# Performance work log

Hardware: AMD Instinct MI355X
Metric: run time of the kernel (lower is better)

## Reference

```python
import jax, jax.numpy as jnp
import numpy as np

D_MODEL = 1024
NUM_HEADS = 16
D_K = D_MODEL // NUM_HEADS
SCALE = float(np.sqrt(D_K))


def setup_inputs() -> dict:
    key = jax.random.key(0)
    ks = jax.random.split(key, 11)
    B, S, D = 2, 2048, D_MODEL
    def lin(kw):
        # xavier-uniform-ish weight, zero bias (matches torch init style)
        lim = float(np.sqrt(6.0 / (D + D)))
        return jax.random.uniform(kw, (D, D), jnp.float32, -lim, lim)
    return {
        "q": jax.random.normal(ks[0], (B, S, D), jnp.float32),
        "k": jax.random.normal(ks[1], (B, S, D), jnp.float32),
        "v": jax.random.normal(ks[2], (B, S, D), jnp.float32),
        "Wq": lin(ks[3]), "bq": jnp.zeros((D,), jnp.float32),
        "Wk": lin(ks[4]), "bk": jnp.zeros((D,), jnp.float32),
        "Wv": lin(ks[5]), "bv": jnp.zeros((D,), jnp.float32),
        "Wo": lin(ks[6]), "bo": jnp.zeros((D,), jnp.float32),
    }


def _split_heads(x):
    B, S, _ = x.shape
    return x.reshape(B, S, NUM_HEADS, D_K).transpose(0, 2, 1, 3)  # (B,H,S,dk)


def reference(q, k, v, Wq, bq, Wk, bk, Wv, bv, Wo, bo):
    # torch nn.Linear: y = x @ W.T + b
    Q = _split_heads(q @ Wq.T + bq)
    K = _split_heads(k @ Wk.T + bk)
    V = _split_heads(v @ Wv.T + bv)
    scores = jnp.einsum("bhqd,bhkd->bhqk", Q, K) / SCALE
    # numerically-stable softmax with detached max (as in the torch code)
    m = jax.lax.stop_gradient(jnp.max(scores, axis=-1, keepdims=True))
    exp_scores = jnp.exp(scores - m)
    attn = exp_scores / (jnp.sum(exp_scores, axis=-1, keepdims=True) + 1e-9)
    out = jnp.einsum("bhqk,bhkd->bhqd", attn, V)  # (B,H,S,dk)
    B, H, S, dk = out.shape
    out = out.transpose(0, 2, 1, 3).reshape(B, S, H * dk)
    return out @ Wo.T + bo
```

## Files before the change

### kernel.cpp

```cpp
#include <hip/hip_runtime.h>


#define D_MODEL 1024
#define NHEADS  16
#define DKH     64
#define SEQ     2048
#define BATCH   2
#define MTOT    (BATCH * SEQ)
#define XE      ((long)MTOT * D_MODEL)
#define WE      ((long)D_MODEL * D_MODEL)
#define QSCALE  0.18033688011112042f

typedef __attribute__((ext_vector_type(8))) short short8v;
typedef __attribute__((ext_vector_type(4))) short short4v;
typedef __attribute__((ext_vector_type(4))) float f32x4;

typedef __attribute__((address_space(1))) void as1_void;
typedef __attribute__((address_space(3))) void as3_void;

__device__ __forceinline__ void gload16(const void* g, void* l) {
    __builtin_amdgcn_global_load_lds((const as1_void*)g, (as3_void*)l, 16, 0, 0);
}

__device__ __forceinline__ unsigned short f2bf(float x) {
    unsigned int u = __float_as_uint(x);
    u += 0x7FFFu + ((u >> 16) & 1u);
    return (unsigned short)(u >> 16);
}

__device__ __forceinline__ float fexp2(float x) {
    return __builtin_amdgcn_exp2f(x);
}

__device__ __forceinline__ unsigned int cvt_pk_bf16(float lo, float hi) {
    unsigned int r;
    asm("v_cvt_pk_bf16_f32 %0, %1, %2" : "=v"(r) : "v"(lo), "v"(hi));
    return r;
}

__device__ __forceinline__ int swz_u(int row, int col) {
    int byte = (col << 1) ^ ((row & 7) << 4);
    return (row << 6) + (byte >> 1);
}

__device__ __forceinline__ int swz_v(int d, int kv) {
    int slot = (d & 6) | ((d >> 3) & 1);
    int byte = (kv << 1) ^ (slot << 4);
    return (d << 6) + (byte >> 1);
}

struct ConvArgs {
    const float*    src[7];
    unsigned short* dst[7];
    int             n4[7];
};

__global__ __launch_bounds__(256) void convert_kernel(ConvArgs a) {
    int z = blockIdx.y;
    const float4*   s = (const float4*)a.src[z];
    unsigned short* d = a.dst[z];
    int n = a.n4[z];
    for (int i = blockIdx.x * blockDim.x + threadIdx.x; i < n;
         i += gridDim.x * blockDim.x) {
        float4 v = s[i];
        ushort4 o;
        o.x = f2bf(v.x); o.y = f2bf(v.y); o.z = f2bf(v.z); o.w = f2bf(v.w);
        *(ushort4*)(d + 4L * i) = o;
    }
}

__device__ __forceinline__ void stv(float* p, float v)          { *p = v; }
__device__ __forceinline__ void stv(unsigned short* p, float v) { *p = f2bf(v); }

template <typename OutT>
__device__ __forceinline__ void gemm_core(const unsigned short* __restrict__ A,
                                          const unsigned short* __restrict__ Bm,
                                          const float* __restrict__ bias,
                                          OutT* __restrict__ C,
                                          int K, int N, float scale) {
    __shared__ unsigned short As[128 * 32];
    __shared__ unsigned short Bs[128 * 32];

    const int t    = threadIdx.x;
    const int lane = t & 63;
    const int w    = t >> 6;
    const int wm   = w >> 1, wn = w & 1;
    const int l15  = lane & 15, g = lane >> 4;
    const long m0  = (long)blockIdx.y * 128;
    const long n0  = (long)blockIdx.x * 128;

    f32x4 acc[4][4] = {};

    const int idx0 = t, idx1 = t + 256;
    const int r0 = idx0 >> 2, c0 = (idx0 & 3) * 8;
    const int r1 = idx1 >> 2, c1 = (idx1 & 3) * 8;
    const unsigned short* pa0 = A  + (m0 + r0) * K + c0;
    const unsigned short* pa1 = A  + (m0 + r1) * K + c1;
    const unsigned short* pb0 = Bm + (n0 + r0) * K + c0;
    const unsigned short* pb1 = Bm + (n0 + r1) * K + c1;

    for (int k0 = 0; k0 < K; k0 += 32) {
        gload16(pa0 + k0, &As[idx0 * 8]);
        gload16(pa1 + k0, &As[idx1 * 8]);
        gload16(pb0 + k0, &Bs[idx0 * 8]);
        gload16(pb1 + k0, &Bs[idx1 * 8]);
        __syncthreads();

        short8v af[4], bf_[4];
#pragma unroll
        for (int mf = 0; mf < 4; ++mf)
            af[mf] = *(const short8v*)&As[(wm * 64 + mf * 16 + l15) * 32 + g * 8];
#pragma unroll
        for (int nf = 0; nf < 4; ++nf)
            bf_[nf] = *(const short8v*)&Bs[(wn * 64 + nf * 16 + l15) * 32 + g * 8];
#pragma unroll
        for (int mf = 0; mf < 4; ++mf)
#pragma unroll
            for (int nf = 0; nf < 4; ++nf)
                acc[mf][nf] = __builtin_amdgcn_mfma_f32_16x16x32_bf16(
                    af[mf], bf_[nf], acc[mf][nf], 0, 0, 0);
        __syncthreads();
    }

    float bvv[4];
#pragma unroll
    for (int nf = 0; nf < 4; ++nf)
        bvv[nf] = bias[n0 + wn * 64 + nf * 16 + l15];

#pragma unroll
    for (int mf = 0; mf < 4; ++mf)
#pragma unroll
        for (int nf = 0; nf < 4; ++nf)
#pragma unroll
            for (int r = 0; r < 4; ++r) {
                long row = m0 + wm * 64 + mf * 16 + g * 4 + r;
                long col = n0 + wn * 64 + nf * 16 + l15;
                float v = (acc[mf][nf][r] + bvv[nf]) * scale;
                stv(C + row * (long)N + col, v);
            }
}

__global__ __launch_bounds__(256) void proj_kernel(
    const unsigned short* __restrict__ xb, const unsigned short* __restrict__ wb,
    const float* __restrict__ bq, const float* __restrict__ bk,
    const float* __restrict__ bv, unsigned short* __restrict__ qkv) {
    int z = blockIdx.z;
    const float* bias = (z == 0) ? bq : (z == 1) ? bk : bv;
    float scale = (z == 0) ? QSCALE : 1.0f;
    gemm_core<unsigned short>(xb + (long)z * XE, wb + (long)z * WE, bias,
                              qkv + (long)z * XE, D_MODEL, D_MODEL, scale);
}

__global__ __launch_bounds__(256) void out_kernel(
    const unsigned short* __restrict__ ob, const unsigned short* __restrict__ wo,
    const float* __restrict__ bo, float* __restrict__ out) {
    gemm_core<float>(ob, wo, bo, out, D_MODEL, D_MODEL, 1.0f);
}

#define KVB 4096

__global__ __launch_bounds__(512) void attn_kernel(
    const unsigned short* __restrict__ Qb, const unsigned short* __restrict__ Kb,
    const unsigned short* __restrict__ Vb, unsigned short* __restrict__ Ob) {
    __shared__ alignas(16) unsigned short Ks[2 * KVB];
    __shared__ alignas(16) unsigned short Vt[2 * KVB];
    __shared__ alignas(16) unsigned short Ps[8][16 * 64];
    __shared__ alignas(16) float corrS[8][16];

    const int t = threadIdx.x, lane = t & 63, w = t >> 6;
    const int l15 = lane & 15, g = lane >> 4;
    const int bh = blockIdx.y;
    const long headoff = (long)(bh >> 4) * SEQ * D_MODEL + (long)(bh & 15) * DKH;
    const int q0w = blockIdx.x * 128 + w * 16;

    short8v qf[2];
#pragma unroll
    for (int ks = 0; ks < 2; ++ks)
        qf[ks] = *(const short8v*)(Qb + headoff +
            (long)(q0w + l15) * D_MODEL + ks * 32 + g * 8);

    short8v onesv;
#pragma unroll
    for (int j = 0; j < 8; ++j) onesv[j] = (short)0x3F80;

    f32x4 o[4] = {};
    f32x4 ol = {};
    float mrun = -3.0e38f;

    const int vd0  = (t & 31) * 2;
    const int vkv0 = (t >> 5) * 4;
    const int kr0 = t >> 3, ks0 = t & 7;

    unsigned int va[4];

#define ISSUE_V(kt)                                                        \
    _Pragma("unroll")                                                      \
    for (int j = 0; j < 4; ++j)                                            \
        va[j] = *(const unsigned int*)(Vb + headoff +                      \
            (long)((kt) + vkv0 + j) * D_MODEL + vd0);

#define ISSUE_K(kt, off)                                                   \
    gload16(Kb + headoff + (long)((kt) + kr0) * D_MODEL +                  \
                ((ks0 ^ (kr0 & 7)) << 3), &Ks[(off) + t * 8]);

#define WRITE_V(off)                                                       \
    {                                                                      \
        short4v ra, rb;                                                    \
        _Pragma("unroll")                                                  \
        for (int j = 0; j < 4; ++j) {                                      \
            ra[j] = (short)(va[j] & 0xffffu);                              \
            rb[j] = (short)(va[j] >> 16);                                  \
        }                                                                  \
        *(short4v*)&Vt[(off) + swz_v(vd0,     vkv0)] = ra;                 \
        *(short4v*)&Vt[(off) + swz_v(vd0 + 1, vkv0)] = rb;                 \
    }

    asm volatile("s_waitcnt vmcnt(0)" ::: "memory");
    ISSUE_V(0);
    ISSUE_K(0, 0);
    WRITE_V(0);
    int cur = 0;

    for (int it = 0; it < SEQ / 64; ++it) {
        const int nxt = cur ^ 1;
        const int ktn = (((it + 1) & (SEQ / 64 - 1))) * 64;
        ISSUE_V(ktn);
        ISSUE_K(ktn, nxt * KVB);
        asm volatile("s_waitcnt vmcnt(5)" ::: "memory");
        asm volatile("s_waitcnt lgkmcnt(0)" ::: "memory");
        __builtin_amdgcn_sched_barrier(0);
        __builtin_amdgcn_s_barrier();
        __builtin_amdgcn_sched_barrier(0);

        const int kO = cur * KVB;

        f32x4 st[4] = {};
        __builtin_amdgcn_s_setprio(1);
#pragma unroll
        for (int ks = 0; ks < 2; ++ks)
#pragma unroll
            for (int mf = 0; mf < 4; ++mf) {
                short8v kf = *(const short8v*)&Ks[kO + swz_u(mf * 16 + l15, ks * 32 + g * 8)];
                st[mf] = __builtin_amdgcn_mfma_f32_16x16x32_bf16(
                    kf, qf[ks], st[mf], 0, 0, 0);
            }
        __builtin_amdgcn_s_setprio(0);

        float vmax = st[0][0];
#pragma unroll
        for (int mf = 0; mf < 4; ++mf)
#pragma unroll
            for (int r = 0; r < 4; ++r)
                vmax = fmaxf(vmax, st[mf][r]);
        vmax = fmaxf(vmax, __shfl_xor(vmax, 16));
        vmax = fmaxf(vmax, __shfl_xor(vmax, 32));

        const bool grow = __any(vmax > mrun + 8.0f);
        if (grow) {
            float mnew = fmaxf(mrun, vmax);
            float corr = fexp2(mrun - mnew);
            mrun = mnew;
            if (g == 0) corrS[w][l15] = corr;
        }

#pragma unroll
        for (int mf = 0; mf < 4; ++mf)
#pragma unroll
            for (int r = 0; r < 4; ++r)
                st[mf][r] = fexp2(st[mf][r] - mrun);

        unsigned short* Pw = Ps[w];
#pragma unroll
        for (int mf = 0; mf < 4; ++mf) {
            uint2 pk;
            pk.x = cvt_pk_bf16(st[mf][0], st[mf][1]);
            pk.y = cvt_pk_bf16(st[mf][2], st[mf][3]);
            *(uint2*)&Pw[swz_u(l15, mf * 16 + g * 4)] = pk;
        }

        if (grow) {
            float4 cv = *(const float4*)&corrS[w][g * 4];
#pragma unroll
            for (int nd = 0; nd < 4; ++nd)
#pragma unroll
                for (int r = 0; r < 4; ++r)
                    o[nd][r] *= cv[r];
#pragma unroll
            for (int r = 0; r < 4; ++r) ol[r] *= cv[r];
        }

        __builtin_amdgcn_s_setprio(1);
#pragma unroll
        for (int ks2 = 0; ks2 < 2; ++ks2) {
            short8v pf = *(const short8v*)&Pw[swz_u(l15, ks2 * 32 + g * 8)];
            ol = __builtin_amdgcn_mfma_f32_16x16x32_bf16(
                pf, onesv, ol, 0, 0, 0);
#pragma unroll
            for (int nd = 0; nd < 4; ++nd) {
                short8v vf = *(const short8v*)&Vt[kO + swz_v(nd * 16 + l15, ks2 * 32 + g * 8)];
                o[nd] = __builtin_amdgcn_mfma_f32_16x16x32_bf16(
                    pf, vf, o[nd], 0, 0, 0);
            }
        }
        __builtin_amdgcn_s_setprio(0);

        WRITE_V(nxt * KVB);
        cur = nxt;
    }

#pragma unroll
    for (int r = 0; r < 4; ++r) {
        float inv = 1.f / (ol[r] + 1e-9f);
        long rowoff = headoff + (long)(q0w + g * 4 + r) * D_MODEL;
#pragma unroll
        for (int nd = 0; nd < 4; ++nd)
            Ob[rowoff + nd * 16 + l15] = f2bf(o[nd][r] * inv);
    }
#undef ISSUE_V
#undef ISSUE_K
#undef WRITE_V
}

extern "C" void kernel_launch(void* const* d_in, const int* in_sizes, int n_in,
                              void* d_out, int out_size, void* d_ws, size_t ws_size,
                              hipStream_t stream) {
    unsigned short* ws  = (unsigned short*)d_ws;
    unsigned short* xb  = ws;
    unsigned short* wb  = ws + 3L * XE;
    unsigned short* qkv = ws + 3L * XE + 4L * WE;
    unsigned short* ob  = qkv + 3L * XE;

    ConvArgs ca;
    ca.src[0] = (const float*)d_in[0]; ca.dst[0] = xb;           ca.n4[0] = (int)(XE / 4);
    ca.src[1] = (const float*)d_in[1]; ca.dst[1] = xb + XE;      ca.n4[1] = (int)(XE / 4);
    ca.src[2] = (const float*)d_in[2]; ca.dst[2] = xb + 2L * XE; ca.n4[2] = (int)(XE / 4);
    ca.src[3] = (const float*)d_in[3]; ca.dst[3] = wb;           ca.n4[3] = (int)(WE / 4);
    ca.src[4] = (const float*)d_in[5]; ca.dst[4] = wb + WE;      ca.n4[4] = (int)(WE / 4);
    ca.src[5] = (const float*)d_in[7]; ca.dst[5] = wb + 2L * WE; ca.n4[5] = (int)(WE / 4);
    ca.src[6] = (const float*)d_in[9]; ca.dst[6] = wb + 3L * WE; ca.n4[6] = (int)(WE / 4);

    hipLaunchKernelGGL(convert_kernel, dim3(512, 7), dim3(256), 0, stream, ca);

    hipLaunchKernelGGL(proj_kernel, dim3(8, 32, 3), dim3(256), 0, stream,
                       xb, wb, (const float*)d_in[4], (const float*)d_in[6],
                       (const float*)d_in[8], qkv);

    hipLaunchKernelGGL(attn_kernel, dim3(16, 32), dim3(512), 0, stream,
                       qkv, qkv + XE, qkv + 2L * XE, ob);

    hipLaunchKernelGGL(out_kernel, dim3(8, 32), dim3(256), 0, stream,
                       ob, wb + 3L * WE, (const float*)d_in[10], (float*)d_out);
}
```

Baseline: 140.9 us.

## Switch attention to 32x32x16 MFMA with 32-row waves and permlane P reuse

Rewrites the attention kernel around 32x32x16 bf16 MFMA tiles. Each wave now owns 32 query rows and the block drops to 256 threads. The P matrix no longer makes a round trip through LDS: it is rearranged in registers with v_permlane32_swap and fed straight into the PV MFMA, which also removes the Ps shared buffer. The goal is fewer LDS transactions and higher MFMA throughput per wave, at the cost of more accumulator registers and fewer waves per block to hide latency.

```diff
diff --git a/kernel.cpp b/kernel.cpp
--- a/kernel.cpp
+++ b/kernel.cpp
@@ -11,9 +11,10 @@
 #define WE      ((long)D_MODEL * D_MODEL)
 #define QSCALE  0.18033688011112042f
 
-typedef __attribute__((ext_vector_type(8))) short short8v;
-typedef __attribute__((ext_vector_type(4))) short short4v;
-typedef __attribute__((ext_vector_type(4))) float f32x4;
+typedef __attribute__((ext_vector_type(8)))  short short8v;
+typedef __attribute__((ext_vector_type(4)))  short short4v;
+typedef __attribute__((ext_vector_type(4)))  float f32x4;
+typedef __attribute__((ext_vector_type(16))) float f32x16;
 
 typedef __attribute__((address_space(1))) void as1_void;
 typedef __attribute__((address_space(3))) void as3_void;
@@ -159,60 +160,62 @@
 
 #define KVB 4096
 
-__global__ __launch_bounds__(512) void attn_kernel(
+__global__ __launch_bounds__(256) void attn_kernel(
     const unsigned short* __restrict__ Qb, const unsigned short* __restrict__ Kb,
     const unsigned short* __restrict__ Vb, unsigned short* __restrict__ Ob) {
     __shared__ alignas(16) unsigned short Ks[2 * KVB];
     __shared__ alignas(16) unsigned short Vt[2 * KVB];
-    __shared__ alignas(16) unsigned short Ps[8][16 * 64];
-    __shared__ alignas(16) float corrS[8][16];
+    __shared__ alignas(16) float corrS[4][32];
 
     const int t = threadIdx.x, lane = t & 63, w = t >> 6;
-    const int l15 = lane & 15, g = lane >> 4;
+    const int l31 = lane & 31, h = lane >> 5;
     const int bh = blockIdx.y;
     const long headoff = (long)(bh >> 4) * SEQ * D_MODEL + (long)(bh & 15) * DKH;
-    const int q0w = blockIdx.x * 128 + w * 16;
-
-    short8v qf[2];
-#pragma unroll
-    for (int ks = 0; ks < 2; ++ks)
-        qf[ks] = *(const short8v*)(Qb + headoff +
-            (long)(q0w + l15) * D_MODEL + ks * 32 + g * 8);
+    const int q0w = blockIdx.x * 128 + w * 32;
+
+    short8v qf[4];
+#pragma unroll
+    for (int step = 0; step < 4; ++step)
+        qf[step] = *(const short8v*)(Qb + headoff +
+            (long)(q0w + l31) * D_MODEL + step * 16 + h * 8);
 
     short8v onesv;
 #pragma unroll
     for (int j = 0; j < 8; ++j) onesv[j] = (short)0x3F80;
 
-    f32x4 o[4] = {};
-    f32x4 ol = {};
+    f32x16 o[2] = {};
+    f32x16 ol = {};
     float mrun = -3.0e38f;
 
     const int vd0  = (t & 31) * 2;
-    const int vkv0 = (t >> 5) * 4;
-    const int kr0 = t >> 3, ks0 = t & 7;
-
-    unsigned int va[4];
+    const int vkv0 = (t >> 5) * 8;
+    const int kr0 = t >> 3,         ks0  = t & 7;
+    const int kr1 = (t + 256) >> 3, ks1_ = (t + 256) & 7;
+
+    unsigned int va[8];
 
 #define ISSUE_V(kt)                                                        \
     _Pragma("unroll")                                                      \
-    for (int j = 0; j < 4; ++j)                                            \
+    for (int j = 0; j < 8; ++j)                                            \
         va[j] = *(const unsigned int*)(Vb + headoff +                      \
             (long)((kt) + vkv0 + j) * D_MODEL + vd0);
 
 #define ISSUE_K(kt, off)                                                   \
     gload16(Kb + headoff + (long)((kt) + kr0) * D_MODEL +                  \
-                ((ks0 ^ (kr0 & 7)) << 3), &Ks[(off) + t * 8]);
+                ((ks0 ^ (kr0 & 7)) << 3), &Ks[(off) + t * 8]);             \
+    gload16(Kb + headoff + (long)((kt) + kr1) * D_MODEL +                  \
+                ((ks1_ ^ (kr1 & 7)) << 3), &Ks[(off) + (t + 256) * 8]);
 
 #define WRITE_V(off)                                                       \
     {                                                                      \
-        short4v ra, rb;                                                    \
+        short8v ra, rb;                                                    \
         _Pragma("unroll")                                                  \
-        for (int j = 0; j < 4; ++j) {                                      \
+        for (int j = 0; j < 8; ++j) {                                      \
             ra[j] = (short)(va[j] & 0xffffu);                              \
             rb[j] = (short)(va[j] >> 16);                                  \
         }                                                                  \
-        *(short4v*)&Vt[(off) + swz_v(vd0,     vkv0)] = ra;                 \
-        *(short4v*)&Vt[(off) + swz_v(vd0 + 1, vkv0)] = rb;                 \
+        *(short8v*)&Vt[(off) + swz_v(vd0,     vkv0)] = ra;                 \
+        *(short8v*)&Vt[(off) + swz_v(vd0 + 1, vkv0)] = rb;                 \
     }
 
     asm volatile("s_waitcnt vmcnt(0)" ::: "memory");
@@ -223,10 +226,10 @@
 
     for (int it = 0; it < SEQ / 64; ++it) {
         const int nxt = cur ^ 1;
-        const int ktn = (((it + 1) & (SEQ / 64 - 1))) * 64;
+        const int ktn = ((it + 1) & (SEQ / 64 - 1)) * 64;
         ISSUE_V(ktn);
         ISSUE_K(ktn, nxt * KVB);
-        asm volatile("s_waitcnt vmcnt(5)" ::: "memory");
+        asm volatile("s_waitcnt vmcnt(10)" ::: "memory");
         asm volatile("s_waitcnt lgkmcnt(0)" ::: "memory");
         __builtin_amdgcn_sched_barrier(0);
         __builtin_amdgcn_s_barrier();
@@ -234,25 +237,23 @@
 
         const int kO = cur * KVB;
 
-        f32x4 st[4] = {};
+        f32x16 st[2] = {};
         __builtin_amdgcn_s_setprio(1);
 #pragma unroll
-        for (int ks = 0; ks < 2; ++ks)
-#pragma unroll
-            for (int mf = 0; mf < 4; ++mf) {
-                short8v kf = *(const short8v*)&Ks[kO + swz_u(mf * 16 + l15, ks * 32 + g * 8)];
-                st[mf] = __builtin_amdgcn_mfma_f32_16x16x32_bf16(
-                    kf, qf[ks], st[mf], 0, 0, 0);
-            }
+        for (int step = 0; step < 4; ++step) {
+            short8v kf0 = *(const short8v*)&Ks[kO + swz_u(l31,      step * 16 + h * 8)];
+            st[0] = __builtin_amdgcn_mfma_f32_32x32x16_bf16(kf0, qf[step], st[0], 0, 0, 0);
+            short8v kf1 = *(const short8v*)&Ks[kO + swz_u(32 + l31, step * 16 + h * 8)];
+            st[1] = __builtin_amdgcn_mfma_f32_32x32x16_bf16(kf1, qf[step], st[1], 0, 0, 0);
+        }
         __builtin_amdgcn_s_setprio(0);
 
         float vmax = st[0][0];
 #pragma unroll
-        for (int mf = 0; mf < 4; ++mf)
-#pragma unroll
-            for (int r = 0; r < 4; ++r)
-                vmax = fmaxf(vmax, st[mf][r]);
-        vmax = fmaxf(vmax, __shfl_xor(vmax, 16));
+        for (int b = 0; b < 2; ++b)
+#pragma unroll
+            for (int r = 0; r < 16; ++r)
+                vmax = fmaxf(vmax, st[b][r]);
         vmax = fmaxf(vmax, __shfl_xor(vmax, 32));
 
         const bool grow = __any(vmax > mrun + 8.0f);
@@ -260,48 +261,47 @@
             float mnew = fmaxf(mrun, vmax);
             float corr = fexp2(mrun - mnew);
             mrun = mnew;
-            if (g == 0) corrS[w][l15] = corr;
+            if (lane < 32) corrS[w][l31] = corr;
         }
 
 #pragma unroll
-        for (int mf = 0; mf < 4; ++mf)
-#pragma unroll
-            for (int r = 0; r < 4; ++r)
-                st[mf][r] = fexp2(st[mf][r] - mrun);
-
-        unsigned short* Pw = Ps[w];
-#pragma unroll
-        for (int mf = 0; mf < 4; ++mf) {
-            uint2 pk;
-            pk.x = cvt_pk_bf16(st[mf][0], st[mf][1]);
-            pk.y = cvt_pk_bf16(st[mf][2], st[mf][3]);
-            *(uint2*)&Pw[swz_u(l15, mf * 16 + g * 4)] = pk;
-        }
+        for (int b = 0; b < 2; ++b)
+#pragma unroll
+            for (int r = 0; r < 16; ++r)
+                st[b][r] = fexp2(st[b][r] - mrun);
 
         if (grow) {
-            float4 cv = *(const float4*)&corrS[w][g * 4];
-#pragma unroll
-            for (int nd = 0; nd < 4; ++nd)
-#pragma unroll
-                for (int r = 0; r < 4; ++r)
-                    o[nd][r] *= cv[r];
-#pragma unroll
-            for (int r = 0; r < 4; ++r) ol[r] *= cv[r];
-        }
-
-        __builtin_amdgcn_s_setprio(1);
-#pragma unroll
-        for (int ks2 = 0; ks2 < 2; ++ks2) {
-            short8v pf = *(const short8v*)&Pw[swz_u(l15, ks2 * 32 + g * 8)];
-            ol = __builtin_amdgcn_mfma_f32_16x16x32_bf16(
-                pf, onesv, ol, 0, 0, 0);
-#pragma unroll
-            for (int nd = 0; nd < 4; ++nd) {
-                short8v vf = *(const short8v*)&Vt[kO + swz_v(nd * 16 + l15, ks2 * 32 + g * 8)];
-                o[nd] = __builtin_amdgcn_mfma_f32_16x16x32_bf16(
-                    pf, vf, o[nd], 0, 0, 0);
+#pragma unroll
+            for (int q2 = 0; q2 < 4; ++q2) {
+                float4 cv = *(const float4*)&corrS[w][q2 * 8 + h * 4];
+#pragma unroll
+                for (int r3 = 0; r3 < 4; ++r3) {
+                    o[0][q2 * 4 + r3] *= cv[r3];
+                    o[1][q2 * 4 + r3] *= cv[r3];
+                    ol[q2 * 4 + r3]   *= cv[r3];
+                }
             }
         }
+
+        __builtin_amdgcn_s_setprio(1);
+#pragma unroll
+        for (int b = 0; b < 2; ++b)
+#pragma unroll
+            for (int s = 0; s < 2; ++s) {
+                unsigned int u  = cvt_pk_bf16(st[b][s * 8 + 0], st[b][s * 8 + 1]);
+                unsigned int u2 = cvt_pk_bf16(st[b][s * 8 + 2], st[b][s * 8 + 3]);
+                unsigned int v  = cvt_pk_bf16(st[b][s * 8 + 4], st[b][s * 8 + 5]);
+                unsigned int v2 = cvt_pk_bf16(st[b][s * 8 + 6], st[b][s * 8 + 7]);
+                asm("v_permlane32_swap_b32 %0, %1" : "+v"(u),  "+v"(v));
+                asm("v_permlane32_swap_b32 %0, %1" : "+v"(u2), "+v"(v2));
+                uint4 pu = {u, u2, v, v2};
+                short8v pa = __builtin_bit_cast(short8v, pu);
+                ol = __builtin_amdgcn_mfma_f32_32x32x16_bf16(pa, onesv, ol, 0, 0, 0);
+                short8v vb0 = *(const short8v*)&Vt[kO + swz_v(l31,      b * 32 + s * 16 + h * 8)];
+                o[0] = __builtin_amdgcn_mfma_f32_32x32x16_bf16(pa, vb0, o[0], 0, 0, 0);
+                short8v vb1 = *(const short8v*)&Vt[kO + swz_v(32 + l31, b * 32 + s * 16 + h * 8)];
+                o[1] = __builtin_amdgcn_mfma_f32_32x32x16_bf16(pa, vb1, o[1], 0, 0, 0);
+            }
         __builtin_amdgcn_s_setprio(0);
 
         WRITE_V(nxt * KVB);
@@ -309,13 +309,15 @@
     }
 
 #pragma unroll
-    for (int r = 0; r < 4; ++r) {
-        float inv = 1.f / (ol[r] + 1e-9f);
-        long rowoff = headoff + (long)(q0w + g * 4 + r) * D_MODEL;
-#pragma unroll
-        for (int nd = 0; nd < 4; ++nd)
-            Ob[rowoff + nd * 16 + l15] = f2bf(o[nd][r] * inv);
-    }
+    for (int q2 = 0; q2 < 4; ++q2)
+#pragma unroll
+        for (int r3 = 0; r3 < 4; ++r3) {
+            float inv = 1.f / (ol[q2 * 4 + r3] + 1e-9f);
+            long rowoff = headoff +
+                (long)(q0w + q2 * 8 + h * 4 + r3) * D_MODEL;
+            Ob[rowoff + l31]      = f2bf(o[0][q2 * 4 + r3] * inv);
+            Ob[rowoff + 32 + l31] = f2bf(o[1][q2 * 4 + r3] * inv);
+        }
 #undef ISSUE_V
 #undef ISSUE_K
 #undef WRITE_V
@@ -345,7 +347,7 @@
                        xb, wb, (const float*)d_in[4], (const float*)d_in[6],
                        (const float*)d_in[8], qkv);
 
-    hipLaunchKernelGGL(attn_kernel, dim3(16, 32), dim3(512), 0, stream,
+    hipLaunchKernelGGL(attn_kernel, dim3(16, 32), dim3(256), 0, stream,
                        qkv, qkv + XE, qkv + 2L * XE, ob);
 
     hipLaunchKernelGGL(out_kernel, dim3(8, 32), dim3(256), 0, stream,
```

Measured after the change: 143.5 us. About the same (+1.8%).
